# Kernel optimization log

Hardware: AMD Instinct MI355X
Metric: run time of the kernel (lower is better)

The kernel has to match this reference:

```python
import jax, jax.numpy as jnp
import numpy as np

T, B, D, H = 128, 128, 1024, 1024

def setup_inputs() -> dict:
    key = jax.random.key(0)
    ks = jax.random.split(key, 3)
    x = jax.random.normal(ks[0], (T, B, D), jnp.float32)
    reset = (jax.random.uniform(ks[1], (T, B)) < 0.05).astype(jnp.float32)
    h0 = jnp.zeros((1, B, H), jnp.float32)
    c0 = jnp.zeros((1, B, H), jnp.float32)
    W = jax.random.normal(ks[2], (D + H, 4 * H), jnp.float32) / np.float32(np.sqrt(D + H))
    b = jnp.zeros((4 * H,), jnp.float32)
    return {"x": x, "h0": h0, "c0": c0, "reset": reset, "W": W, "b": b}

def _lstm_scan(x, h0, c0, reset, W, b):
    Hh = h0.shape[-1]
    def step(carry, inp):
        h, c = carry
        x_t, r_t = inp
        m = (1.0 - r_t)[:, None]           # reset wipes state
        h = h * m
        c = c * m
        gated = jnp.concatenate([x_t, h], axis=-1) @ W + b  # [B, 4H]
        i, g, f, o = jnp.split(gated, 4, axis=-1)
        f = jax.nn.sigmoid(f + 1.0)        # forget-gate bias of +1 as in source
        c = f * c + jax.nn.sigmoid(i) * jnp.tanh(g)
        h = jax.nn.sigmoid(o) * jnp.tanh(c)
        return (h, c), h
    (hT, cT), ys = jax.lax.scan(step, (h0[0], c0[0]), (x, reset))
    # torch.cat(outputs, dim=0) on per-step [B,H] slices -> [T*B, H]
    out = ys.reshape(-1, Hh)
    return out, hT, cT

def reference(x, h0, c0, reset, W, b):
    out, hT, cT = _lstm_scan(x, h0, c0, reset, W, b)
    return out, hT[None], cT[None]
```

## Files before the change

### kernel.cpp

```cpp
#include <hip/hip_runtime.h>
#include <math.h>

#define T_STEPS 128
#define B_SZ 128
#define D_SZ 1024
#define H_SZ 1024
#define G4 4096
#define KW 2048

typedef __attribute__((ext_vector_type(8))) short bf16x8;
typedef __attribute__((ext_vector_type(4))) float f32x4;
typedef unsigned short ushort_t;
typedef unsigned int uint_t;
typedef unsigned long long ull_t;

__device__ __forceinline__ float sigf(float x) { return 1.0f / (1.0f + __expf(-x)); }
__device__ __forceinline__ float tanhfast(float x) { return 1.0f - 2.0f * sigf(-2.0f * x); }

__device__ __forceinline__ ushort_t f2bf(float f) {
  uint_t u = __float_as_uint(f);
  return (ushort_t)((u + 0x7fffu + ((u >> 16) & 1u)) >> 16);
}
__device__ __forceinline__ float bf2f(ushort_t s) {
  return __uint_as_float(((uint_t)s) << 16);
}

#define GLOAD_LDS16(gp, lp)                                                  \
  __builtin_amdgcn_global_load_lds(                                          \
      (const __attribute__((address_space(1))) unsigned int*)(const void*)(gp), \
      (__attribute__((address_space(3))) unsigned int*)(void*)(lp), 16, 0, 0)

__global__ __launch_bounds__(256) void convert_x(const float* __restrict__ x,
                                                 ushort_t* __restrict__ xbf) {
  const size_t i8 = ((size_t)blockIdx.x * 256 + threadIdx.x) * 8;
  if (i8 + 8 > (size_t)T_STEPS * B_SZ * D_SZ) return;
  float4 a = *(const float4*)&x[i8];
  float4 b = *(const float4*)&x[i8 + 4];
  ushort_t o[8] = {f2bf(a.x), f2bf(a.y), f2bf(a.z), f2bf(a.w),
                   f2bf(b.x), f2bf(b.y), f2bf(b.z), f2bf(b.w)};
  *(uint4*)&xbf[i8] = *(uint4*)o;
}

__global__ __launch_bounds__(256) void transpose_w(const float* __restrict__ W,
                                                   ushort_t* __restrict__ WT) {
  __shared__ float t[32][33];
  const int tx = threadIdx.x & 31;
  const int ty = threadIdx.x >> 5;
  const int k0 = blockIdx.x * 32;
  const int n0 = blockIdx.y * 32;
#pragma unroll
  for (int i = 0; i < 4; ++i)
    t[ty + i * 8][tx] = W[(size_t)(k0 + ty + i * 8) * G4 + n0 + tx];
  __syncthreads();
#pragma unroll
  for (int i = 0; i < 4; ++i)
    WT[(size_t)(n0 + ty + i * 8) * KW + k0 + tx] = f2bf(t[tx][ty + i * 8]);
}

__global__ __launch_bounds__(256) void init_state(const float* __restrict__ h0,
                                                  const float* __restrict__ reset0,
                                                  ushort_t* __restrict__ hbf0) {
  const int i = blockIdx.x * 256 + threadIdx.x;
  if (i >= B_SZ * H_SZ) return;
  hbf0[i] = f2bf(h0[i] * (1.0f - reset0[i >> 10]));
}

__global__ __launch_bounds__(256) void xw_mfma2(const ushort_t* __restrict__ xbf,
                                                const ushort_t* __restrict__ WT,
                                                const float* __restrict__ bias,
                                                ushort_t* __restrict__ xwg) {
  __shared__ ushort_t Asb[2][128 * 64];
  __shared__ ushort_t Bsb[2][128 * 64];

  const int bid = blockIdx.x;
  const int swz = (bid & 7) * 512 + (bid >> 3);
  const int nt = swz >> 7;
  const int mt = swz & 127;
  const int m0 = mt * 128, n0 = nt * 128;
  const int tid = threadIdx.x, lane = tid & 63, wid = tid >> 6;
  const int wr = wid >> 1, wc = wid & 1;
  const int lr = lane & 15, ko = lane >> 4;
  const int srow = lane >> 3;
  const int skb = (lane & 7) * 16;

  f32x4 acc[4][4] = {};

#define XW_STAGE(buf, kt)                                                      \
  {                                                                            \
    const int k0b = (kt) * 128;                                                \
    _Pragma("unroll") for (int i = 0; i < 4; ++i) {                            \
      const int c = wid * 4 + i;                                               \
      const int row = c * 8 + srow;                                            \
      const int sw = skb ^ ((row & 7) << 4);                                   \
      GLOAD_LDS16((const char*)xbf + (size_t)(m0 + row) * 2048 + k0b + sw,     \
                  (char*)&Asb[buf][0] + c * 1024);                             \
      GLOAD_LDS16((const char*)WT + (size_t)(n0 + row) * 4096 + k0b + sw,      \
                  (char*)&Bsb[buf][0] + c * 1024);                             \
    }                                                                          \
  }

  XW_STAGE(0, 0);
  __syncthreads();
  const int xsw = (lr & 7) << 4;
  for (int kt = 0; kt < 16; ++kt) {
    if (kt + 1 < 16) XW_STAGE((kt + 1) & 1, kt + 1);
    const char* Ab = (const char*)&Asb[kt & 1][0] + (wr * 64 + lr) * 128;
    const char* Bb = (const char*)&Bsb[kt & 1][0] + (wc * 64 + lr) * 128;
#pragma unroll
    for (int ks = 0; ks < 2; ++ks) {
      const int kb = (ks * 64 + ko * 16) ^ xsw;
      bf16x8 a[4], b[4];
#pragma unroll
      for (int mi = 0; mi < 4; ++mi) a[mi] = *(const bf16x8*)(Ab + mi * 2048 + kb);
#pragma unroll
      for (int ni = 0; ni < 4; ++ni) b[ni] = *(const bf16x8*)(Bb + ni * 2048 + kb);
#pragma unroll
      for (int mi = 0; mi < 4; ++mi)
#pragma unroll
        for (int ni = 0; ni < 4; ++ni)
          acc[mi][ni] = __builtin_amdgcn_mfma_f32_16x16x32_bf16(a[mi], b[ni], acc[mi][ni], 0, 0, 0);
    }
    __syncthreads();
  }

  const int rr = ko * 4;
#pragma unroll
  for (int ni = 0; ni < 4; ++ni) {
    const int n = n0 + wc * 64 + ni * 16 + lr;
    const int gg = n >> 10;
    const int jj = n & 1023;
    const float bn = bias[n];
#pragma unroll
    for (int mi = 0; mi < 4; ++mi) {
#pragma unroll
      for (int r = 0; r < 4; ++r) {
        const int m = m0 + wr * 64 + mi * 16 + rr + r;
        const int tt = m >> 7;
        const int btp = (m & 127) >> 5;
        const int r32 = m & 31;
        xwg[((((size_t)tt * 4 + btp) * 64 + (jj >> 4)) * 512 + r32 * 16 + (jj & 15)) * 4 + gg] =
            f2bf(acc[mi][ni][r] + bn);
      }
    }
  }
}

__global__ __launch_bounds__(512) void lstm_persist5(
    const ushort_t* __restrict__ hbf0,
    const float* __restrict__ c0,
    const float* __restrict__ reset,
    const ushort_t* __restrict__ xwg,
    const ushort_t* __restrict__ WT,
    float* __restrict__ out,
    ushort_t* __restrict__ hring,
    uint_t* __restrict__ bar)
{
  __shared__ ushort_t WhL[64 * 512];
  __shared__ ushort_t Ah[32 * 1024];
  __shared__ float sc[2][4][16][17];

  const int tid = threadIdx.x;
  const int bid = blockIdx.x;
  const int jt = bid & 63;
  const int btp = bid >> 6;
  const int b0 = btp * 32;
  const int lane = tid & 63;
  const int wid = tid >> 6;
  const int g = wid & 3;
  const int mh = wid >> 2;
  const int lr = lane & 15;
  const int ko = lane >> 4;
  const size_t SE = (size_t)B_SZ * H_SZ;

  uint_t* const arr = bar + btp * 256;

  for (int p = 0; p < 8; ++p) {
    const int id = p * 512 + tid;
    const int wrw = id >> 6;
    const int kb = (id & 63) * 16;
    const int n = (wrw >> 4) * H_SZ + jt * 16 + (wrw & 15);
    const uint4 v = *(const uint4*)((const char*)WT + (size_t)n * 4096 + 2048 + kb);
    *(uint4*)((char*)WhL + wrw * 1024 + (kb ^ ((wrw & 7) << 4))) = v;
  }

  const char* wrow = (const char*)WT + (size_t)(g * H_SZ + jt * 16 + lr) * 4096;
  bf16x8 breg[16];
#pragma unroll
  for (int q = 0; q < 16; ++q)
    breg[q] = *(const bf16x8*)(wrow + 3072 + q * 64 + ko * 16);

  const int row = tid >> 4;
  const int col = tid & 15;
  const int b = b0 + row;
  const int j = jt * 16 + col;
  const size_t so = (size_t)b * H_SZ + j;
  float creg = c0[so] * (1.0f - reset[b]);

  const int swzl = (lr & 7) << 4;
  const char* aBase = (const char*)Ah + (mh * 16 + lr) * 2048;
  const char* bBase = (const char*)WhL + (g * 16 + lr) * 1024;

  ull_t xwv = *(const ull_t*)(xwg + (((size_t)btp * 64 + jt) * 512 + tid) * 4);
  float mn = 1.0f - reset[B_SZ + b];

  for (int t = 0; t < T_STEPS; ++t) {
    const char* hsrc = (t == 0) ? (const char*)hbf0
                                : (const char*)(hring + (size_t)t * SE);
#pragma unroll
    for (int i = 0; i < 8; ++i) {
      const int c = wid * 8 + i;
      const int hrow = c >> 1;
      const int half = (c & 1) * 1024;
      const int kb = half + lane * 16;
      const int src = kb ^ ((hrow & 7) << 4);
      GLOAD_LDS16(hsrc + (size_t)(b0 + hrow) * 2048 + src,
                  (char*)Ah + hrow * 2048 + half);
    }
    __syncthreads();

    f32x4 acc = {};
#pragma unroll
    for (int ks = 0; ks < 16; ++ks) {
      bf16x8 a = *(const bf16x8*)(aBase + ((ks * 64 + ko * 16) ^ swzl));
      bf16x8 bb = *(const bf16x8*)(bBase + ((ks * 64 + ko * 16) ^ swzl));
      acc = __builtin_amdgcn_mfma_f32_16x16x32_bf16(a, bb, acc, 0, 0, 0);
    }
#pragma unroll
    for (int ks = 0; ks < 16; ++ks) {
      bf16x8 a = *(const bf16x8*)(aBase + (((16 + ks) * 64 + ko * 16) ^ swzl));
      acc = __builtin_amdgcn_mfma_f32_16x16x32_bf16(a, breg[ks], acc, 0, 0, 0);
    }
#pragma unroll
    for (int r = 0; r < 4; ++r) sc[mh][g][ko * 4 + r][lr] = acc[r];
    __syncthreads();

    const float gi = sc[row >> 4][0][row & 15][col] + bf2f((ushort_t)xwv);
    const float gg = sc[row >> 4][1][row & 15][col] + bf2f((ushort_t)(xwv >> 16));
    const float gf = sc[row >> 4][2][row & 15][col] + bf2f((ushort_t)(xwv >> 32));
    const float go = sc[row >> 4][3][row & 15][col] + bf2f((ushort_t)(xwv >> 48));
    const float f = sigf(gf + 1.0f);
    const float cn = f * creg + sigf(gi) * tanhfast(gg);
    const float hn = sigf(go) * tanhfast(cn);
    out[(size_t)t * SE + so] = hn;
    creg = cn * mn;

    if (t < T_STEPS - 1) {
      __hip_atomic_store(hring + (size_t)(t + 1) * SE + so, f2bf(hn * mn),
                         __ATOMIC_RELAXED, __HIP_MEMORY_SCOPE_AGENT);
      asm volatile("s_waitcnt vmcnt(0)" ::: "memory");
      __syncthreads();

      if (tid == 0)
        __hip_atomic_store(&arr[jt], (uint_t)(t + 1),
                           __ATOMIC_RELAXED, __HIP_MEMORY_SCOPE_AGENT);

      xwv = *(const ull_t*)(xwg + ((((size_t)(t + 1) * 4 + btp) * 64 + jt) * 512 + tid) * 4);
      mn = (t + 1 < T_STEPS - 1) ? (1.0f - reset[(size_t)(t + 2) * B_SZ + b]) : 1.0f;

      if (wid == 0) {
        uint_t it = 0;
        for (;;) {
          const uint_t v = __hip_atomic_load(&arr[lane], __ATOMIC_RELAXED,
                                             __HIP_MEMORY_SCOPE_AGENT);
          if (__all((int)v > t)) break;
          __builtin_amdgcn_s_sleep(1);
          if (++it > 1000000u) break;
        }
      }
      __syncthreads();
    } else {
      float* hT = out + (size_t)T_STEPS * SE;
      float* cT = hT + SE;
      hT[so] = hn;
      cT[so] = cn;
    }
  }
}

extern "C" void kernel_launch(void* const* d_in, const int* in_sizes, int n_in,
                              void* d_out, int out_size, void* d_ws, size_t ws_size,
                              hipStream_t stream) {
  (void)in_sizes; (void)n_in; (void)out_size; (void)ws_size;
  const float* x = (const float*)d_in[0];
  const float* h0 = (const float*)d_in[1];
  const float* c0 = (const float*)d_in[2];
  const float* reset = (const float*)d_in[3];
  const float* W = (const float*)d_in[4];
  const float* bias = (const float*)d_in[5];
  float* out = (float*)d_out;

  const size_t TB = (size_t)T_STEPS * B_SZ;
  const size_t SE = (size_t)B_SZ * H_SZ;

  char* p = (char*)d_ws;
  uint_t* bar = (uint_t*)p;               p += 4096;
  ushort_t* WT = (ushort_t*)p;            p += (size_t)G4 * KW * 2;
  ushort_t* xbf = (ushort_t*)p;           p += TB * D_SZ * 2;
  ushort_t* xwg = (ushort_t*)p;           p += TB * G4 * 2;
  ushort_t* hbf0 = (ushort_t*)p;          p += SE * 2;
  ushort_t* hring = (ushort_t*)p;         p += (size_t)T_STEPS * SE * 2;

  hipMemsetAsync(bar, 0, 4096, stream);
  convert_x<<<dim3((int)(TB * D_SZ / 8 / 256)), 256, 0, stream>>>(x, xbf);
  transpose_w<<<dim3(KW / 32, G4 / 32), 256, 0, stream>>>(W, WT);
  init_state<<<dim3((int)((SE + 255) / 256)), 256, 0, stream>>>(h0, reset, hbf0);
  xw_mfma2<<<dim3(4096), 256, 0, stream>>>(xbf, WT, bias, xwg);

  lstm_persist5<<<dim3(256), 512, 0, stream>>>(hbf0, c0, reset, xwg, WT, out, hring, bar);
}
```

Baseline: 884.1 us.

## Retile XW GEMM per XCD, vectorize stores, split MFMA chains, restructure barrier wait

```diff
diff --git a/kernel.cpp b/kernel.cpp
--- a/kernel.cpp
+++ b/kernel.cpp
@@ -65,7 +65,7 @@
   hbf0[i] = f2bf(h0[i] * (1.0f - reset0[i >> 10]));
 }
 
-__global__ __launch_bounds__(256) void xw_mfma2(const ushort_t* __restrict__ xbf,
+__global__ __launch_bounds__(256) void xw_mfma3(const ushort_t* __restrict__ xbf,
                                                 const ushort_t* __restrict__ WT,
                                                 const float* __restrict__ bias,
                                                 ushort_t* __restrict__ xwg) {
@@ -73,9 +73,10 @@
   __shared__ ushort_t Bsb[2][128 * 64];
 
   const int bid = blockIdx.x;
-  const int swz = (bid & 7) * 512 + (bid >> 3);
-  const int nt = swz >> 7;
-  const int mt = swz & 127;
+  const int xcd = bid & 7;
+  const int ib = bid >> 3;
+  const int mt = (ib >> 5) * 8 + (ib & 7);
+  const int nt = xcd * 4 + ((ib >> 3) & 3);
   const int m0 = mt * 128, n0 = nt * 128;
   const int tid = threadIdx.x, lane = tid & 63, wid = tid >> 6;
   const int wr = wid >> 1, wc = wid & 1;
@@ -127,25 +128,25 @@
 #pragma unroll
   for (int ni = 0; ni < 4; ++ni) {
     const int n = n0 + wc * 64 + ni * 16 + lr;
-    const int gg = n >> 10;
-    const int jj = n & 1023;
+    const int g = n >> 10;
+    const int jtn = (n & 1023) >> 4;
     const float bn = bias[n];
 #pragma unroll
     for (int mi = 0; mi < 4; ++mi) {
-#pragma unroll
-      for (int r = 0; r < 4; ++r) {
-        const int m = m0 + wr * 64 + mi * 16 + rr + r;
-        const int tt = m >> 7;
-        const int btp = (m & 127) >> 5;
-        const int r32 = m & 31;
-        xwg[((((size_t)tt * 4 + btp) * 64 + (jj >> 4)) * 512 + r32 * 16 + (jj & 15)) * 4 + gg] =
-            f2bf(acc[mi][ni][r] + bn);
-      }
-    }
-  }
-}
-
-__global__ __launch_bounds__(512) void lstm_persist5(
+      const int m = m0 + wr * 64 + mi * 16 + rr;
+      const int tt = m >> 7;
+      const int btp = (m & 127) >> 5;
+      const int r32 = m & 31;
+      ushort_t tmp[4];
+#pragma unroll
+      for (int r = 0; r < 4; ++r) tmp[r] = f2bf(acc[mi][ni][r] + bn);
+      *(ull_t*)(xwg + (((size_t)tt * 4 + btp) * 64 + jtn) * 2048 + g * 512 + lr * 32 + r32) =
+          *(ull_t*)tmp;
+    }
+  }
+}
+
+__global__ __launch_bounds__(512) void lstm_persist6(
     const ushort_t* __restrict__ hbf0,
     const float* __restrict__ c0,
     const float* __restrict__ reset,
@@ -200,10 +201,24 @@
   const char* aBase = (const char*)Ah + (mh * 16 + lr) * 2048;
   const char* bBase = (const char*)WhL + (g * 16 + lr) * 1024;
 
-  ull_t xwv = *(const ull_t*)(xwg + (((size_t)btp * 64 + jt) * 512 + tid) * 4);
+  ushort_t xq0, xq1, xq2, xq3;
+  {
+    const ushort_t* xp = xwg + (((size_t)btp) * 64 + jt) * 2048 + col * 32 + row;
+    xq0 = xp[0]; xq1 = xp[512]; xq2 = xp[1024]; xq3 = xp[1536];
+  }
   float mn = 1.0f - reset[B_SZ + b];
 
   for (int t = 0; t < T_STEPS; ++t) {
+    if (t > 0) {
+      uint_t it = 0;
+      for (;;) {
+        const uint_t v = __hip_atomic_load(&arr[lane], __ATOMIC_RELAXED,
+                                           __HIP_MEMORY_SCOPE_AGENT);
+        if (__all((int)v >= t)) break;
+        __builtin_amdgcn_s_sleep(1);
+        if (++it > 1000000u) break;
+      }
+    }
     const char* hsrc = (t == 0) ? (const char*)hbf0
                                 : (const char*)(hring + (size_t)t * SE);
 #pragma unroll
@@ -218,26 +233,42 @@
     }
     __syncthreads();
 
-    f32x4 acc = {};
-#pragma unroll
-    for (int ks = 0; ks < 16; ++ks) {
-      bf16x8 a = *(const bf16x8*)(aBase + ((ks * 64 + ko * 16) ^ swzl));
-      bf16x8 bb = *(const bf16x8*)(bBase + ((ks * 64 + ko * 16) ^ swzl));
-      acc = __builtin_amdgcn_mfma_f32_16x16x32_bf16(a, bb, acc, 0, 0, 0);
-    }
-#pragma unroll
-    for (int ks = 0; ks < 16; ++ks) {
-      bf16x8 a = *(const bf16x8*)(aBase + (((16 + ks) * 64 + ko * 16) ^ swzl));
-      acc = __builtin_amdgcn_mfma_f32_16x16x32_bf16(a, breg[ks], acc, 0, 0, 0);
-    }
+    f32x4 ac0 = {}, ac1 = {}, ac2 = {}, ac3 = {};
+#pragma unroll
+    for (int q = 0; q < 4; ++q) {
+      bf16x8 a0 = *(const bf16x8*)(aBase + (((q * 4 + 0) * 64 + ko * 16) ^ swzl));
+      bf16x8 b0f = *(const bf16x8*)(bBase + (((q * 4 + 0) * 64 + ko * 16) ^ swzl));
+      ac0 = __builtin_amdgcn_mfma_f32_16x16x32_bf16(a0, b0f, ac0, 0, 0, 0);
+      bf16x8 a1 = *(const bf16x8*)(aBase + (((q * 4 + 1) * 64 + ko * 16) ^ swzl));
+      bf16x8 b1f = *(const bf16x8*)(bBase + (((q * 4 + 1) * 64 + ko * 16) ^ swzl));
+      ac1 = __builtin_amdgcn_mfma_f32_16x16x32_bf16(a1, b1f, ac1, 0, 0, 0);
+      bf16x8 a2 = *(const bf16x8*)(aBase + (((q * 4 + 2) * 64 + ko * 16) ^ swzl));
+      bf16x8 b2f = *(const bf16x8*)(bBase + (((q * 4 + 2) * 64 + ko * 16) ^ swzl));
+      ac2 = __builtin_amdgcn_mfma_f32_16x16x32_bf16(a2, b2f, ac2, 0, 0, 0);
+      bf16x8 a3 = *(const bf16x8*)(aBase + (((q * 4 + 3) * 64 + ko * 16) ^ swzl));
+      bf16x8 b3f = *(const bf16x8*)(bBase + (((q * 4 + 3) * 64 + ko * 16) ^ swzl));
+      ac3 = __builtin_amdgcn_mfma_f32_16x16x32_bf16(a3, b3f, ac3, 0, 0, 0);
+    }
+#pragma unroll
+    for (int q = 0; q < 4; ++q) {
+      bf16x8 a0 = *(const bf16x8*)(aBase + (((16 + q * 4 + 0) * 64 + ko * 16) ^ swzl));
+      ac0 = __builtin_amdgcn_mfma_f32_16x16x32_bf16(a0, breg[q * 4 + 0], ac0, 0, 0, 0);
+      bf16x8 a1 = *(const bf16x8*)(aBase + (((16 + q * 4 + 1) * 64 + ko * 16) ^ swzl));
+      ac1 = __builtin_amdgcn_mfma_f32_16x16x32_bf16(a1, breg[q * 4 + 1], ac1, 0, 0, 0);
+      bf16x8 a2 = *(const bf16x8*)(aBase + (((16 + q * 4 + 2) * 64 + ko * 16) ^ swzl));
+      ac2 = __builtin_amdgcn_mfma_f32_16x16x32_bf16(a2, breg[q * 4 + 2], ac2, 0, 0, 0);
+      bf16x8 a3 = *(const bf16x8*)(aBase + (((16 + q * 4 + 3) * 64 + ko * 16) ^ swzl));
+      ac3 = __builtin_amdgcn_mfma_f32_16x16x32_bf16(a3, breg[q * 4 + 3], ac3, 0, 0, 0);
+    }
+    const f32x4 acc = (ac0 + ac1) + (ac2 + ac3);
 #pragma unroll
     for (int r = 0; r < 4; ++r) sc[mh][g][ko * 4 + r][lr] = acc[r];
     __syncthreads();
 
-    const float gi = sc[row >> 4][0][row & 15][col] + bf2f((ushort_t)xwv);
-    const float gg = sc[row >> 4][1][row & 15][col] + bf2f((ushort_t)(xwv >> 16));
-    const float gf = sc[row >> 4][2][row & 15][col] + bf2f((ushort_t)(xwv >> 32));
-    const float go = sc[row >> 4][3][row & 15][col] + bf2f((ushort_t)(xwv >> 48));
+    const float gi = sc[row >> 4][0][row & 15][col] + bf2f(xq0);
+    const float gg = sc[row >> 4][1][row & 15][col] + bf2f(xq1);
+    const float gf = sc[row >> 4][2][row & 15][col] + bf2f(xq2);
+    const float go = sc[row >> 4][3][row & 15][col] + bf2f(xq3);
     const float f = sigf(gf + 1.0f);
     const float cn = f * creg + sigf(gi) * tanhfast(gg);
     const float hn = sigf(go) * tanhfast(cn);
@@ -245,8 +276,16 @@
     creg = cn * mn;
 
     if (t < T_STEPS - 1) {
-      __hip_atomic_store(hring + (size_t)(t + 1) * SE + so, f2bf(hn * mn),
-                         __ATOMIC_RELAXED, __HIP_MEMORY_SCOPE_AGENT);
+      const uint_t hm = (uint_t)f2bf(hn * mn);
+      const uint_t h1 = (uint_t)__shfl_down((int)hm, 1);
+      const uint_t h2 = (uint_t)__shfl_down((int)hm, 2);
+      const uint_t h3 = (uint_t)__shfl_down((int)hm, 3);
+      if ((col & 3) == 0) {
+        const ull_t pk = (ull_t)(hm & 0xffffu) | ((ull_t)(h1 & 0xffffu) << 16) |
+                         ((ull_t)(h2 & 0xffffu) << 32) | ((ull_t)(h3 & 0xffffu) << 48);
+        __hip_atomic_store((ull_t*)(hring + (size_t)(t + 1) * SE + so), pk,
+                           __ATOMIC_RELAXED, __HIP_MEMORY_SCOPE_AGENT);
+      }
       asm volatile("s_waitcnt vmcnt(0)" ::: "memory");
       __syncthreads();
 
@@ -254,20 +293,9 @@
         __hip_atomic_store(&arr[jt], (uint_t)(t + 1),
                            __ATOMIC_RELAXED, __HIP_MEMORY_SCOPE_AGENT);
 
-      xwv = *(const ull_t*)(xwg + ((((size_t)(t + 1) * 4 + btp) * 64 + jt) * 512 + tid) * 4);
+      const ushort_t* xp = xwg + (((size_t)(t + 1) * 4 + btp) * 64 + jt) * 2048 + col * 32 + row;
+      xq0 = xp[0]; xq1 = xp[512]; xq2 = xp[1024]; xq3 = xp[1536];
       mn = (t + 1 < T_STEPS - 1) ? (1.0f - reset[(size_t)(t + 2) * B_SZ + b]) : 1.0f;
-
-      if (wid == 0) {
-        uint_t it = 0;
-        for (;;) {
-          const uint_t v = __hip_atomic_load(&arr[lane], __ATOMIC_RELAXED,
-                                             __HIP_MEMORY_SCOPE_AGENT);
-          if (__all((int)v > t)) break;
-          __builtin_amdgcn_s_sleep(1);
-          if (++it > 1000000u) break;
-        }
-      }
-      __syncthreads();
     } else {
       float* hT = out + (size_t)T_STEPS * SE;
       float* cT = hT + SE;
@@ -304,7 +332,7 @@
   convert_x<<<dim3((int)(TB * D_SZ / 8 / 256)), 256, 0, stream>>>(x, xbf);
   transpose_w<<<dim3(KW / 32, G4 / 32), 256, 0, stream>>>(W, WT);
   init_state<<<dim3((int)((SE + 255) / 256)), 256, 0, stream>>>(h0, reset, hbf0);
-  xw_mfma2<<<dim3(4096), 256, 0, stream>>>(xbf, WT, bias, xwg);
-
-  lstm_persist5<<<dim3(256), 512, 0, stream>>>(hbf0, c0, reset, xwg, WT, out, hring, bar);
-}
+  xw_mfma3<<<dim3(4096), 256, 0, stream>>>(xbf, WT, bias, xwg);
+
+  lstm_persist6<<<dim3(256), 512, 0, stream>>>(hbf0, c0, reset, xwg, WT, out, hring, bar);
+}
```

After: 768.9 us. 13.0% less time.
